# Kernel optimization log

Hardware: AMD Instinct MI355X
Metric: run time of the kernel (lower is better)

Reference implementation:

```python
import jax, jax.numpy as jnp
import numpy as np

NUM_USERS = 100000
NUM_BOOKS = 50000
HIDDEN = 128
USER_FEAT = 256
BOOK_FEAT = 256
E_PER_REL = 500000
NUM_LAYERS = 2


def setup_inputs() -> dict:
    key = jax.random.key(0)
    ks = jax.random.split(key, 10)
    user_x = jax.random.normal(ks[0], (NUM_USERS, USER_FEAT), dtype=jnp.float32)
    book_x = jax.random.normal(ks[1], (NUM_BOOKS, BOOK_FEAT), dtype=jnp.float32)
    user_W = jax.random.normal(ks[2], (HIDDEN, USER_FEAT), dtype=jnp.float32) * 0.05
    user_b = jax.random.normal(ks[3], (HIDDEN,), dtype=jnp.float32) * 0.05
    book_W = jax.random.normal(ks[4], (HIDDEN, BOOK_FEAT), dtype=jnp.float32) * 0.05
    book_b = jax.random.normal(ks[5], (HIDDEN,), dtype=jnp.float32) * 0.05
    # edge_index[0] = user indices, edge_index[1] = book indices
    rates_edge = jnp.stack([
        jax.random.randint(ks[6], (E_PER_REL,), 0, NUM_USERS),
        jax.random.randint(ks[7], (E_PER_REL,), 0, NUM_BOOKS)])
    implicit_edge = jnp.stack([
        jax.random.randint(ks[8], (E_PER_REL,), 0, NUM_USERS),
        jax.random.randint(ks[9], (E_PER_REL,), 0, NUM_BOOKS)])
    return {"user_x": user_x, "book_x": book_x, "user_W": user_W,
            "user_b": user_b, "book_W": book_W, "book_b": book_b,
            "rates_edge": rates_edge, "implicit_edge": implicit_edge}


def _lightgcn(user_x, book_x, user_W, user_b, book_W, book_b, rates_edge, implicit_edge):
    num_users = user_x.shape[0]
    num_nodes = num_users + book_x.shape[0]
    # input projections
    cu = user_x @ user_W.T + user_b  # [U, H]
    cb = book_x @ book_W.T + book_b  # [B, H]
    user_embeds = [cu]
    book_embeds = [cb]
    # build full directed edge list exactly as in the torch source
    all_edges = jnp.concatenate([rates_edge, implicit_edge], axis=1)  # [2, E]
    book_to_user = jnp.stack([all_edges[1] + num_users, all_edges[0]])
    full_edge = jnp.concatenate([all_edges, book_to_user], axis=1)  # [2, 2E]
    row, col = full_edge[0], full_edge[1]
    # symmetric degree normalization (edges fixed across layers)
    deg = jax.ops.segment_sum(jnp.ones(col.shape, dtype=cu.dtype), col,
                              num_segments=num_nodes)
    deg_inv_sqrt = jnp.where(deg > 0, jax.lax.rsqrt(jnp.maximum(deg, 1.0) * 0 + jnp.where(deg > 0, deg, 1.0)), 0.0)
    deg_inv_sqrt = jnp.where(deg > 0, jax.lax.rsqrt(jnp.where(deg > 0, deg, 1.0)), 0.0)
    norm = deg_inv_sqrt[row] * deg_inv_sqrt[col]  # [2E]
    for _ in range(NUM_LAYERS):
        x = jnp.concatenate([cu, cb], axis=0)  # [U+B, H]
        msg = x[row] * norm[:, None]           # gather + scale, [2E, H]
        out = jax.ops.segment_sum(msg, col, num_segments=num_nodes)  # scatter-add
        cu = out[:num_users]
        cb = out[num_users:]
        user_embeds.append(cu)
        book_embeds.append(cb)
    final_user = jnp.mean(jnp.stack(user_embeds), axis=0)
    final_book = jnp.mean(jnp.stack(book_embeds), axis=0)
    return final_user, final_book


def reference(user_x, book_x, user_W, user_b, book_W, book_b, rates_edge, implicit_edge):
    return _lightgcn(user_x, book_x, user_W, user_b, book_W, book_b,
                     rates_edge, implicit_edge)
```

## Files before the change

### kernel.cpp

```cpp
#include <hip/hip_runtime.h>

#define NUSERS 100000
#define NBOOKS 50000
#define HID 128
#define FEAT 256
#define EPR 500000
#define NEDGE (2 * EPR)

#define UBLK64 ((NUSERS + 63) / 64)
#define BBLK64 ((NBOOKS + 63) / 64)
#define GH_BLOCKS (UBLK64 + BBLK64)
#define FILL_B ((NEDGE + 255) / 256)
#define DIS_B ((NUSERS + 255) / 256)

typedef __attribute__((ext_vector_type(8))) short bf16x8;
typedef __attribute__((ext_vector_type(4))) float f32x4;

__device__ __forceinline__ unsigned short f2bf(float f) {
  union { float f; unsigned u; } v; v.f = f;
  unsigned r = v.u + 0x7FFFu + ((v.u >> 16) & 1u);
  return (unsigned short)(r >> 16);
}
__device__ __forceinline__ float bf2f(unsigned short h) {
  union { unsigned u; float f; } v; v.u = ((unsigned)h) << 16;
  return v.f;
}
__device__ __forceinline__ unsigned pk2bf(float lo, float hi) {
  unsigned r;
  asm("v_cvt_pk_bf16_f32 %0, %1, %2" : "=v"(r) : "v"(lo), "v"(hi));
  return r;
}

__global__ void cast_w(const float* __restrict__ w0, const float* __restrict__ w1,
                       unsigned short* __restrict__ o0, unsigned short* __restrict__ o1)
{
  int i = blockIdx.x * 256 + threadIdx.x;
  if (i < HID * FEAT) { o0[i] = f2bf(w0[i]); o1[i] = f2bf(w1[i]); }
}

__device__ __forceinline__ void decode_edge(const int* __restrict__ rates,
                                            const int* __restrict__ impl,
                                            int i, int& u, int& bk)
{
  if (i < EPR) { u = rates[i]; bk = rates[EPR + i]; }
  else { int j = i - EPR; u = impl[j]; bk = impl[EPR + j]; }
}

__global__ __launch_bounds__(256) void gemm_hist(
    const float* __restrict__ Xu, const float* __restrict__ Xb,
    const unsigned short* __restrict__ Wu, const unsigned short* __restrict__ Wb,
    const float* __restrict__ bu, const float* __restrict__ bb,
    unsigned short* __restrict__ cu0b, float* __restrict__ outb,
    float* __restrict__ outu,
    const int* __restrict__ rates, const int* __restrict__ impl,
    int* __restrict__ degu, int* __restrict__ cntb,
    int* __restrict__ relpos)
{
  __shared__ float Asb[4][2048];
  const int bid = blockIdx.x;
  const int tid = threadIdx.x;
  const int lane = tid & 63;
  const int wv   = tid >> 6;
  const int l15  = lane & 15, l4 = lane >> 4;

  const bool isU = bid < UBLK64;
  const float* __restrict__ X = isU ? Xu : Xb;
  const unsigned short* __restrict__ W = isU ? Wu : Wb;
  const float* __restrict__ bias = isU ? bu : bb;
  const int M    = isU ? NUSERS : NBOOKS;
  const int bm   = (isU ? bid : bid - UBLK64) * 64;
  const int wrow = bm + wv * 16;

  float* wbase = &Asb[wv][0];

  f32x4 acc[8];
#pragma unroll
  for (int ni = 0; ni < 8; ++ni) acc[ni] = (f32x4)0.f;

#pragma unroll
  for (int h = 0; h < 2; ++h) {
    if (h) {
      asm volatile("s_waitcnt lgkmcnt(0)" ::: "memory");
      __builtin_amdgcn_sched_barrier(0);
    }
#pragma unroll
    for (int rnd = 0; rnd < 8; ++rnd) {
      int o = rnd * 64 + lane;
      int r = o >> 5;
      int c = o & 31;
      int lc = c ^ r;
      int gr = wrow + r; if (gr > M - 1) gr = M - 1;
      __builtin_amdgcn_global_load_lds(
          (const float*)&X[(size_t)gr * FEAT + h * 128 + lc * 4],
          wbase + rnd * 256, 16, 0, 0);
    }
    asm volatile("s_waitcnt vmcnt(0)" ::: "memory");
    __builtin_amdgcn_sched_barrier(0);

#pragma unroll
    for (int ks = 0; ks < 4; ++ks) {
      const int kg = h * 4 + ks;
      bf16x8 bfr[8];
#pragma unroll
      for (int ni = 0; ni < 8; ++ni)
        bfr[ni] = *reinterpret_cast<const bf16x8*>(
            &W[(size_t)(ni * 16 + l15) * FEAT + kg * 32 + l4 * 8]);

      int u0 = (ks * 8 + l4 * 2) ^ l15;
      int u1 = (ks * 8 + l4 * 2 + 1) ^ l15;
      f32x4 a0 = *reinterpret_cast<const f32x4*>(&wbase[(l15 * 32 + u0) * 4]);
      f32x4 a1 = *reinterpret_cast<const f32x4*>(&wbase[(l15 * 32 + u1) * 4]);
      union { unsigned u32[4]; bf16x8 v; } au;
      au.u32[0] = pk2bf(a0[0], a0[1]);
      au.u32[1] = pk2bf(a0[2], a0[3]);
      au.u32[2] = pk2bf(a1[0], a1[1]);
      au.u32[3] = pk2bf(a1[2], a1[3]);

#pragma unroll
      for (int ni = 0; ni < 8; ++ni)
        acc[ni] = __builtin_amdgcn_mfma_f32_16x16x32_bf16(au.v, bfr[ni], acc[ni], 0, 0, 0);
    }
  }

#pragma unroll
  for (int ni = 0; ni < 8; ++ni) {
    int col = ni * 16 + l15;
    float bj = bias[col];
#pragma unroll
    for (int j = 0; j < 4; ++j) {
      int rr = wrow + l4 * 4 + j;
      if (rr < M) {
        float vv = acc[ni][j] + bj;
        if (isU) {
          cu0b[(size_t)rr * HID + col] = f2bf(vv);
          if (rr >= NBOOKS) outu[(size_t)rr * HID + col] = vv * (1.0f / 3.0f);
        } else {
          outb[(size_t)rr * HID + col] = vv * (1.0f / 3.0f);
        }
      }
    }
  }

  const int e0 = bid * 512 + tid;
  const int e1 = e0 + 256;
  if (e0 < NEDGE) {
    int u, bk;
    decode_edge(rates, impl, e0, u, bk);
    int p0 = atomicAdd(&cntb[bk], 1);
    atomicAdd(&degu[u], 1);
    relpos[e0] = p0;
  }
  if (e1 < NEDGE) {
    int u, bk;
    decode_edge(rates, impl, e1, u, bk);
    int p1 = atomicAdd(&cntb[bk], 1);
    atomicAdd(&degu[u], 1);
    relpos[e1] = p1;
  }
}

__global__ void fill_dis(const int* __restrict__ rates, const int* __restrict__ impl,
                         const int* __restrict__ offs,
                         const int* __restrict__ relpos,
                         int* __restrict__ brow,
                         const int* __restrict__ degu, const int* __restrict__ cntb,
                         float* __restrict__ dis)
{
  int b = blockIdx.x;
  if (b >= FILL_B) {
    int i = (b - FILL_B) * 256 + threadIdx.x;
    if (i < NUSERS) {
      int d = degu[i] + (i < NBOOKS ? cntb[i] : 0);
      dis[i] = (d > 0) ? rsqrtf((float)d) : 0.f;
    }
    return;
  }
  int i = b * 256 + threadIdx.x;
  if (i >= NEDGE) return;
  int u, bk;
  decode_edge(rates, impl, i, u, bk);
  brow[offs[bk] + relpos[i]] = u;
}

__global__ __launch_bounds__(1024) void scan_blocks(const int* __restrict__ counts,
                                                    int* __restrict__ offs,
                                                    int* __restrict__ bsum, int N)
{
  __shared__ int buf[1024];
  int t = threadIdx.x;
  int i = blockIdx.x * 1024 + t;
  int v = (i < N) ? counts[i] : 0;
  buf[t] = v;
  __syncthreads();
  for (int off = 1; off < 1024; off <<= 1) {
    int x = (t >= off) ? buf[t - off] : 0;
    __syncthreads();
    buf[t] += x;
    __syncthreads();
  }
  int incl = buf[t];
  if (i < N) offs[i] = incl - v;
  if (t == 1023) bsum[blockIdx.x] = incl;
}

__global__ void scan_totals(const int* __restrict__ bsum, int* __restrict__ bpre,
                            int* __restrict__ offs, int nb, int N)
{
  if (threadIdx.x == 0 && blockIdx.x == 0) {
    int run = 0;
    for (int b = 0; b < nb; ++b) { bpre[b] = run; run += bsum[b]; }
    offs[N] = run;
  }
}

__global__ void add_prefix(int* __restrict__ offs, const int* __restrict__ bpre, int N)
{
  int i = blockIdx.x * blockDim.x + threadIdx.x;
  if (i < N) offs[i] += bpre[i >> 10];
}

__global__ __launch_bounds__(256) void pull1(const unsigned short* __restrict__ srcb,
    const int* __restrict__ offs, const int* __restrict__ brow,
    const float* __restrict__ dis, unsigned short* __restrict__ dstb)
{
  int c = (blockIdx.x << 2) + (threadIdx.x >> 6);
  if (c >= NBOOKS) return;
  const int lane = threadIdx.x & 63;
  const int g = lane >> 4, l = lane & 15;
  const int s = offs[c], e = offs[c + 1];

  float acc[8];
#pragma unroll
  for (int j = 0; j < 8; ++j) acc[j] = 0.f;

  int i = s + g;
  for (; i + 4 < e; i += 8) {
    int rr0 = brow[i], rr1 = brow[i + 4];
    float w0 = dis[rr0], w1 = dis[rr1];
    bf16x8 v0 = *reinterpret_cast<const bf16x8*>(&srcb[(size_t)rr0 * HID + l * 8]);
    bf16x8 v1 = *reinterpret_cast<const bf16x8*>(&srcb[(size_t)rr1 * HID + l * 8]);
#pragma unroll
    for (int j = 0; j < 8; ++j) acc[j] += w0 * bf2f((unsigned short)v0[j]);
#pragma unroll
    for (int j = 0; j < 8; ++j) acc[j] += w1 * bf2f((unsigned short)v1[j]);
  }
  if (i < e) {
    int rr = brow[i];
    float w = dis[rr];
    bf16x8 v = *reinterpret_cast<const bf16x8*>(&srcb[(size_t)rr * HID + l * 8]);
#pragma unroll
    for (int j = 0; j < 8; ++j) acc[j] += w * bf2f((unsigned short)v[j]);
  }

#pragma unroll
  for (int j = 0; j < 8; ++j) {
    acc[j] += __shfl_xor(acc[j], 16, 64);
    acc[j] += __shfl_xor(acc[j], 32, 64);
  }
  if (g == 0) {
    float db = dis[c];
    bf16x8 o;
#pragma unroll
    for (int j = 0; j < 8; ++j) o[j] = (short)f2bf(db * acc[j]);
    *reinterpret_cast<bf16x8*>(&dstb[(size_t)c * HID + l * 8]) = o;
  }
}

__global__ __launch_bounds__(256) void pull2_final(const unsigned short* __restrict__ h1b,
    const int* __restrict__ offs, const int* __restrict__ brow,
    const float* __restrict__ dis, const unsigned short* __restrict__ cu0b,
    float* __restrict__ outu)
{
  int c = (blockIdx.x << 2) + (threadIdx.x >> 6);
  if (c >= NBOOKS) return;
  const int lane = threadIdx.x & 63;
  const int g = lane >> 4, l = lane & 15;
  const int s = offs[c], e = offs[c + 1];

  float acc[8];
#pragma unroll
  for (int j = 0; j < 8; ++j) acc[j] = 0.f;

  int i = s + g;
  for (; i + 4 < e; i += 8) {
    int rr0 = brow[i], rr1 = brow[i + 4];
    int rc0 = rr0 < NBOOKS ? rr0 : 0;
    int rc1 = rr1 < NBOOKS ? rr1 : 0;
    float w0 = rr0 < NBOOKS ? dis[rr0] : 0.f;
    float w1 = rr1 < NBOOKS ? dis[rr1] : 0.f;
    bf16x8 v0 = *reinterpret_cast<const bf16x8*>(&h1b[(size_t)rc0 * HID + l * 8]);
    bf16x8 v1 = *reinterpret_cast<const bf16x8*>(&h1b[(size_t)rc1 * HID + l * 8]);
#pragma unroll
    for (int j = 0; j < 8; ++j) acc[j] += w0 * bf2f((unsigned short)v0[j]);
#pragma unroll
    for (int j = 0; j < 8; ++j) acc[j] += w1 * bf2f((unsigned short)v1[j]);
  }
  if (i < e) {
    int rr = brow[i];
    int rc = rr < NBOOKS ? rr : 0;
    float w = rr < NBOOKS ? dis[rr] : 0.f;
    bf16x8 v = *reinterpret_cast<const bf16x8*>(&h1b[(size_t)rc * HID + l * 8]);
#pragma unroll
    for (int j = 0; j < 8; ++j) acc[j] += w * bf2f((unsigned short)v[j]);
  }

#pragma unroll
  for (int j = 0; j < 8; ++j) {
    acc[j] += __shfl_xor(acc[j], 16, 64);
    acc[j] += __shfl_xor(acc[j], 32, 64);
  }
  if (g == 0) {
    float db = dis[c];
    size_t idx = (size_t)c * HID + l * 8;
    bf16x8 c0 = *reinterpret_cast<const bf16x8*>(&cu0b[idx]);
    bf16x8 h1 = *reinterpret_cast<const bf16x8*>(&h1b[idx]);
    float r[8];
#pragma unroll
    for (int j = 0; j < 8; ++j)
      r[j] = (bf2f((unsigned short)c0[j]) + bf2f((unsigned short)h1[j]) + db * acc[j]) * (1.0f / 3.0f);
    *reinterpret_cast<float4*>(&outu[idx])     = make_float4(r[0], r[1], r[2], r[3]);
    *reinterpret_cast<float4*>(&outu[idx + 4]) = make_float4(r[4], r[5], r[6], r[7]);
  }
}

extern "C" void kernel_launch(void* const* d_in, const int* in_sizes, int n_in,
                              void* d_out, int out_size, void* d_ws, size_t ws_size,
                              hipStream_t stream)
{
  const float* user_x = (const float*)d_in[0];
  const float* book_x = (const float*)d_in[1];
  const float* user_W = (const float*)d_in[2];
  const float* user_b = (const float*)d_in[3];
  const float* book_W = (const float*)d_in[4];
  const float* book_b = (const float*)d_in[5];
  const int*   rates  = (const int*)d_in[6];
  const int*   impl   = (const int*)d_in[7];

  float* out      = (float*)d_out;
  float* out_user = out;
  float* out_book = out + (size_t)NUSERS * HID;

  char* p = (char*)d_ws;
  auto carve = [&](size_t bytes) -> void* {
    void* r = (void*)p;
    p += (bytes + 255) & ~(size_t)255;
    return r;
  };
  unsigned short* cu0b   = (unsigned short*)carve((size_t)NUSERS * HID * 2);
  unsigned short* h1b    = (unsigned short*)carve((size_t)NBOOKS * HID * 2);
  unsigned short* wub    = (unsigned short*)carve((size_t)HID * FEAT * 2);
  unsigned short* wbb    = (unsigned short*)carve((size_t)HID * FEAT * 2);
  int*   degu   = (int*)carve((size_t)NUSERS * 4);
  int*   cntb   = (int*)carve((size_t)NBOOKS * 4);
  float* dis    = (float*)carve((size_t)NUSERS * 4);
  int*   offs   = (int*)carve((size_t)(NBOOKS + 2) * 4);
  int*   bsum   = (int*)carve(256 * 4);
  int*   bpre   = (int*)carve(256 * 4);
  int*   relpos = (int*)carve((size_t)NEDGE * 4);
  int*   brow   = (int*)carve((size_t)NEDGE * 4);

  hipMemsetAsync(degu, 0, (size_t)NUSERS * 4, stream);
  hipMemsetAsync(cntb, 0, (size_t)NBOOKS * 4, stream);

  cast_w<<<(HID * FEAT + 255) / 256, 256, 0, stream>>>(user_W, book_W, wub, wbb);

  gemm_hist<<<GH_BLOCKS, 256, 0, stream>>>(
      user_x, book_x, wub, wbb, user_b, book_b,
      cu0b, out_book, out_user, rates, impl, degu, cntb, relpos);

  const int nb = (NBOOKS + 1023) / 1024;
  scan_blocks<<<nb, 1024, 0, stream>>>(cntb, offs, bsum, NBOOKS);
  scan_totals<<<1, 64, 0, stream>>>(bsum, bpre, offs, nb, NBOOKS);
  add_prefix<<<(NBOOKS + 255) / 256, 256, 0, stream>>>(offs, bpre, NBOOKS);

  fill_dis<<<FILL_B + DIS_B, 256, 0, stream>>>(rates, impl, offs, relpos, brow,
                                               degu, cntb, dis);

  pull1<<<(NBOOKS + 3) / 4, 256, 0, stream>>>(cu0b, offs, brow, dis, h1b);
  pull2_final<<<(NBOOKS + 3) / 4, 256, 0, stream>>>(h1b, offs, brow, dis, cu0b, out_user);
}
```

Measured before the change: 275.5 us.

## Privatize edge histogram per XCD using workgroup-scope atomics and merge afterwards

The degree and book-count histograms become eight copies, one per XCD, chosen at runtime from the hardware XCC_ID register. Their atomics drop to workgroup scope, so increments no longer need device-wide coherence across XCDs. The histogram work also moves to the start of the GEMM kernel. A new merge kernel sums the copies, computes deg^-1/2, and turns per-XCD counts into exclusive offsets that the scatter kernel uses to place rows. The costs are larger memsets, an extra launch, and a reliance on workgroup-scope atomics staying coherent across CUs that share an XCD's L2.

Measured after the change: 288.3 us. +4.6%, slower.

```diff
diff --git a/kernel.cpp b/kernel.cpp
--- a/kernel.cpp
+++ b/kernel.cpp
@@ -11,7 +11,7 @@
 #define BBLK64 ((NBOOKS + 63) / 64)
 #define GH_BLOCKS (UBLK64 + BBLK64)
 #define FILL_B ((NEDGE + 255) / 256)
-#define DIS_B ((NUSERS + 255) / 256)
+#define NXCD 8
 
 typedef __attribute__((ext_vector_type(8))) short bf16x8;
 typedef __attribute__((ext_vector_type(4))) float f32x4;
@@ -29,6 +29,11 @@
   unsigned r;
   asm("v_cvt_pk_bf16_f32 %0, %1, %2" : "=v"(r) : "v"(lo), "v"(hi));
   return r;
+}
+__device__ __forceinline__ int xcc_id() {
+  unsigned id;
+  asm volatile("s_getreg_b32 %0, hwreg(HW_REG_XCC_ID)" : "=s"(id));
+  return (int)(id & 7);
 }
 
 __global__ void cast_w(const float* __restrict__ w0, const float* __restrict__ w1,
@@ -53,8 +58,8 @@
     unsigned short* __restrict__ cu0b, float* __restrict__ outb,
     float* __restrict__ outu,
     const int* __restrict__ rates, const int* __restrict__ impl,
-    int* __restrict__ degu, int* __restrict__ cntb,
-    int* __restrict__ relpos)
+    int* __restrict__ degu8, int* __restrict__ cntb8,
+    unsigned* __restrict__ relpos)
 {
   __shared__ float Asb[4][2048];
   const int bid = blockIdx.x;
@@ -62,6 +67,26 @@
   const int lane = tid & 63;
   const int wv   = tid >> 6;
   const int l15  = lane & 15, l4 = lane >> 4;
+
+  {
+    const unsigned x = (unsigned)xcc_id();
+    int* cnt = cntb8 + (size_t)x * NBOOKS;
+    int* deg = degu8 + (size_t)x * NUSERS;
+    const int e0 = bid * 512 + tid;
+#pragma unroll
+    for (int q = 0; q < 2; ++q) {
+      int e = e0 + q * 256;
+      if (e < NEDGE) {
+        int u, bk;
+        decode_edge(rates, impl, e, u, bk);
+        unsigned p = (unsigned)__hip_atomic_fetch_add(&cnt[bk], 1, __ATOMIC_RELAXED,
+                                                      __HIP_MEMORY_SCOPE_WORKGROUP);
+        __hip_atomic_fetch_add(&deg[u], 1, __ATOMIC_RELAXED,
+                               __HIP_MEMORY_SCOPE_WORKGROUP);
+        relpos[e] = (x << 29) | (p & 0x1FFFFFFFu);
+      }
+    }
+  }
 
   const bool isU = bid < UBLK64;
   const float* __restrict__ X = isU ? Xu : Xb;
@@ -140,46 +165,44 @@
       }
     }
   }
-
-  const int e0 = bid * 512 + tid;
-  const int e1 = e0 + 256;
-  if (e0 < NEDGE) {
-    int u, bk;
-    decode_edge(rates, impl, e0, u, bk);
-    int p0 = atomicAdd(&cntb[bk], 1);
-    atomicAdd(&degu[u], 1);
-    relpos[e0] = p0;
-  }
-  if (e1 < NEDGE) {
-    int u, bk;
-    decode_edge(rates, impl, e1, u, bk);
-    int p1 = atomicAdd(&cntb[bk], 1);
-    atomicAdd(&degu[u], 1);
-    relpos[e1] = p1;
-  }
-}
-
-__global__ void fill_dis(const int* __restrict__ rates, const int* __restrict__ impl,
-                         const int* __restrict__ offs,
-                         const int* __restrict__ relpos,
-                         int* __restrict__ brow,
-                         const int* __restrict__ degu, const int* __restrict__ cntb,
-                         float* __restrict__ dis)
-{
-  int b = blockIdx.x;
-  if (b >= FILL_B) {
-    int i = (b - FILL_B) * 256 + threadIdx.x;
-    if (i < NUSERS) {
-      int d = degu[i] + (i < NBOOKS ? cntb[i] : 0);
-      dis[i] = (d > 0) ? rsqrtf((float)d) : 0.f;
-    }
-    return;
-  }
-  int i = b * 256 + threadIdx.x;
+}
+
+__global__ void merge_dis(int* __restrict__ cntb8, const int* __restrict__ degu8,
+                          int* __restrict__ cntb, float* __restrict__ dis)
+{
+  int i = blockIdx.x * 256 + threadIdx.x;
+  if (i >= NUSERS) return;
+  int d = 0;
+#pragma unroll
+  for (int x = 0; x < NXCD; ++x) d += degu8[(size_t)x * NUSERS + i];
+  if (i < NBOOKS) {
+    int run = 0;
+#pragma unroll
+    for (int x = 0; x < NXCD; ++x) {
+      int c = cntb8[(size_t)x * NBOOKS + i];
+      cntb8[(size_t)x * NBOOKS + i] = run;
+      run += c;
+    }
+    cntb[i] = run;
+    d += run;
+  }
+  dis[i] = (d > 0) ? rsqrtf((float)d) : 0.f;
+}
+
+__global__ void fill_scatter(const int* __restrict__ rates, const int* __restrict__ impl,
+                             const int* __restrict__ offs,
+                             const unsigned* __restrict__ relpos,
+                             const int* __restrict__ cntb8,
+                             int* __restrict__ brow)
+{
+  int i = blockIdx.x * 256 + threadIdx.x;
   if (i >= NEDGE) return;
   int u, bk;
   decode_edge(rates, impl, i, u, bk);
-  brow[offs[bk] + relpos[i]] = u;
+  unsigned rp = relpos[i];
+  unsigned x  = (rp >> 29) & 7u;
+  int rel     = (int)(rp & 0x1FFFFFFFu);
+  brow[offs[bk] + cntb8[(size_t)x * NBOOKS + bk] + rel] = u;
 }
 
 __global__ __launch_bounds__(1024) void scan_blocks(const int* __restrict__ counts,
@@ -350,31 +373,33 @@
   unsigned short* h1b    = (unsigned short*)carve((size_t)NBOOKS * HID * 2);
   unsigned short* wub    = (unsigned short*)carve((size_t)HID * FEAT * 2);
   unsigned short* wbb    = (unsigned short*)carve((size_t)HID * FEAT * 2);
-  int*   degu   = (int*)carve((size_t)NUSERS * 4);
-  int*   cntb   = (int*)carve((size_t)NBOOKS * 4);
-  float* dis    = (float*)carve((size_t)NUSERS * 4);
-  int*   offs   = (int*)carve((size_t)(NBOOKS + 2) * 4);
-  int*   bsum   = (int*)carve(256 * 4);
-  int*   bpre   = (int*)carve(256 * 4);
-  int*   relpos = (int*)carve((size_t)NEDGE * 4);
-  int*   brow   = (int*)carve((size_t)NEDGE * 4);
-
-  hipMemsetAsync(degu, 0, (size_t)NUSERS * 4, stream);
-  hipMemsetAsync(cntb, 0, (size_t)NBOOKS * 4, stream);
+  int*      degu8  = (int*)carve((size_t)NXCD * NUSERS * 4);
+  int*      cntb8  = (int*)carve((size_t)NXCD * NBOOKS * 4);
+  int*      cntb   = (int*)carve((size_t)NBOOKS * 4);
+  float*    dis    = (float*)carve((size_t)NUSERS * 4);
+  int*      offs   = (int*)carve((size_t)(NBOOKS + 2) * 4);
+  int*      bsum   = (int*)carve(256 * 4);
+  int*      bpre   = (int*)carve(256 * 4);
+  unsigned* relpos = (unsigned*)carve((size_t)NEDGE * 4);
+  int*      brow   = (int*)carve((size_t)NEDGE * 4);
+
+  hipMemsetAsync(degu8, 0, (size_t)NXCD * NUSERS * 4, stream);
+  hipMemsetAsync(cntb8, 0, (size_t)NXCD * NBOOKS * 4, stream);
 
   cast_w<<<(HID * FEAT + 255) / 256, 256, 0, stream>>>(user_W, book_W, wub, wbb);
 
   gemm_hist<<<GH_BLOCKS, 256, 0, stream>>>(
       user_x, book_x, wub, wbb, user_b, book_b,
-      cu0b, out_book, out_user, rates, impl, degu, cntb, relpos);
+      cu0b, out_book, out_user, rates, impl, degu8, cntb8, relpos);
+
+  merge_dis<<<(NUSERS + 255) / 256, 256, 0, stream>>>(cntb8, degu8, cntb, dis);
 
   const int nb = (NBOOKS + 1023) / 1024;
   scan_blocks<<<nb, 1024, 0, stream>>>(cntb, offs, bsum, NBOOKS);
   scan_totals<<<1, 64, 0, stream>>>(bsum, bpre, offs, nb, NBOOKS);
   add_prefix<<<(NBOOKS + 255) / 256, 256, 0, stream>>>(offs, bpre, NBOOKS);
 
-  fill_dis<<<FILL_B + DIS_B, 256, 0, stream>>>(rates, impl, offs, relpos, brow,
-                                               degu, cntb, dis);
+  fill_scatter<<<FILL_B, 256, 0, stream>>>(rates, impl, offs, relpos, cntb8, brow);
 
   pull1<<<(NBOOKS + 3) / 4, 256, 0, stream>>>(cu0b, offs, brow, dis, h1b);
   pull2_final<<<(NBOOKS + 3) / 4, 256, 0, stream>>>(h1b, offs, brow, dis, cu0b, out_user);
```
